# Kernel optimization log

Measured on AMD Instinct MI355X. Metric: run time of the kernel, lower is better.

## Reference

```python
import jax, jax.numpy as jnp
import numpy as np

B, C, N = 2, 512, 2048
HEADS, DIM_HEAD, SCALE = 16, 64, 8.0
H_DIM = HEADS * DIM_HEAD
EPS = 1e-12  # F.normalize default eps


def setup_inputs() -> dict:
    key = jax.random.key(0)
    ks = jax.random.split(key, 5)
    x = jax.random.normal(ks[0], (B, C, N), dtype=jnp.float32)
    Wqkv = jax.random.normal(ks[1], (3 * H_DIM, C), dtype=jnp.float32) * (1.0 / np.sqrt(C))
    q_scale = jnp.ones((DIM_HEAD,), dtype=jnp.float32)
    k_scale = jnp.ones((DIM_HEAD,), dtype=jnp.float32)
    Wout = jax.random.normal(ks[2], (C, H_DIM), dtype=jnp.float32) * (1.0 / np.sqrt(H_DIM))
    bout = jax.random.normal(ks[3], (C,), dtype=jnp.float32) * 0.01
    return {"x": x, "Wqkv": Wqkv, "q_scale": q_scale, "k_scale": k_scale,
            "Wout": Wout, "bout": bout}


def _l2norm(t):
    # F.normalize(t, dim=-1): t / max(||t||, eps)
    n = jnp.sqrt(jnp.sum(t * t, axis=-1, keepdims=True))
    return t / jnp.maximum(n, EPS)


def reference(x, Wqkv, q_scale, k_scale, Wout, bout):
    # 1x1 conv == pointwise matmul over channel dim
    qkv = jnp.einsum('oc,bcn->bon', Wqkv, x)              # [B, 3*H_DIM, N]
    q, k, v = jnp.split(qkv, 3, axis=1)
    # unflatten channels -> [B, H, D, N]
    def to_heads(t):
        return t.reshape(B, HEADS, DIM_HEAD, N)
    q, k, v = map(to_heads, (q, k, v))
    # cosine attention: l2-normalize q,k over head dim, apply learned per-dim scales
    q = _l2norm(q.transpose(0, 1, 3, 2)) * q_scale        # [B, H, N, D]
    k = _l2norm(k.transpose(0, 1, 3, 2)) * k_scale        # [B, H, N, D]
    sim = jnp.einsum('bhid,bhjd->bhij', q, k) * SCALE     # [B, H, N, N]
    attn = jax.nn.softmax(sim, axis=-1)
    out = jnp.einsum('bhij,bhdj->bhid', attn, v)          # [B, H, N, D]
    out = out.transpose(0, 1, 3, 2).reshape(B, H_DIM, N)  # b h n d -> b (h d) n
    return jnp.einsum('oc,bcn->bon', Wout, out) + bout[None, :, None]
```

## Files before the change

### kernel.cpp

```cpp
#include <hip/hip_runtime.h>
#include <hip/hip_bf16.h>

#define BATCH 2
#define CCH   512
#define NSEQ  2048
#define HEADS 16
#define DHEAD 64
#define HDIM  1024
#define ODIM  3072
#define QK_PRESCALE 11.541560327111707f

typedef short short4v __attribute__((ext_vector_type(4)));
typedef short short8 __attribute__((ext_vector_type(8)));
typedef float float4v __attribute__((ext_vector_type(4)));

__device__ __forceinline__ unsigned short f2bf(float f) {
    unsigned int u = __float_as_uint(f);
    return (unsigned short)((u + 0x7FFFu + ((u >> 16) & 1u)) >> 16);
}
__device__ __forceinline__ unsigned short f2bf_fast(float f) {
    return (unsigned short)((__float_as_uint(f) + 0x8000u) >> 16);
}
__device__ __forceinline__ float fexp2(float x) {
#if __has_builtin(__builtin_amdgcn_exp2f)
    return __builtin_amdgcn_exp2f(x);
#else
    return exp2f(x);
#endif
}

typedef __attribute__((address_space(1))) const void* as1_cvp;
typedef __attribute__((address_space(3))) void* as3_vp;
__device__ __forceinline__ void cp16(const void* g, void* l) {
    __builtin_amdgcn_global_load_lds((as1_cvp)g, (as3_vp)l, 16, 0, 0);
}

__global__ __launch_bounds__(256) void k_prep(
    const float* __restrict__ Wqkv, const float* __restrict__ Wout,
    const float* __restrict__ x,
    const float* __restrict__ qs, const float* __restrict__ ks,
    unsigned short* __restrict__ Wqkvb, unsigned short* __restrict__ Woutb,
    unsigned short* __restrict__ xt, float* __restrict__ M) {
    const int bx = blockIdx.x;
    if (bx < 2048) {
        if (bx == 0 && threadIdx.x < 64) {
            int lane = threadIdx.x;
            float p = fabsf(qs[lane] * ks[lane]);
#pragma unroll
            for (int off = 1; off < 64; off <<= 1) p = fmaxf(p, __shfl_xor(p, off));
            if (lane == 0) *M = QK_PRESCALE * p;
        }
        int i4 = (bx * 256 + threadIdx.x) * 4;
        const float* src; unsigned short* dst; int idx;
        if (i4 < ODIM * CCH) { src = Wqkv; dst = Wqkvb; idx = i4; }
        else { src = Wout; dst = Woutb; idx = i4 - ODIM * CCH; }
        float4 v = *(const float4*)(src + idx);
        ushort4 o;
        o.x = f2bf(v.x); o.y = f2bf(v.y); o.z = f2bf(v.z); o.w = f2bf(v.w);
        *(ushort4*)(dst + idx) = o;
        return;
    }
    __shared__ unsigned short t[64][65];
    const int fx = bx - 2048;
    const int n0 = (fx & 31) * 64;
    const int c0 = ((fx >> 5) & 7) * 64;
    const int b  = fx >> 8;
    const int tr = threadIdx.x >> 6, tc = threadIdx.x & 63;
    const float* xs = x + (size_t)b * CCH * NSEQ;
    unsigned short* xd = xt + (size_t)b * NSEQ * CCH;
#pragma unroll
    for (int r = 0; r < 16; ++r) {
        int c = r * 4 + tr;
        t[c][tc] = f2bf(xs[(size_t)(c0 + c) * NSEQ + n0 + tc]);
    }
    __syncthreads();
#pragma unroll
    for (int r = 0; r < 16; ++r) {
        int n = r * 4 + tr;
        xd[(size_t)(n0 + n) * CCH + c0 + tc] = t[tc][n];
    }
}

__global__ __launch_bounds__(256) void k_gemm_qkv(
    const unsigned short* __restrict__ W, const unsigned short* __restrict__ xt,
    const float* __restrict__ qs, const float* __restrict__ ks,
    unsigned short* __restrict__ qh, unsigned short* __restrict__ kh,
    unsigned short* __restrict__ vb) {
    constexpr int K = CCH, N = NSEQ;
    __shared__ __align__(16) short smem[2 * 128 * 64];
    short* lsA = smem;
    short* lsB = smem + 128 * 64;
    const int tid = threadIdx.x, wave = tid >> 6, lane = tid & 63;
    const int l15 = lane & 15, quad = lane >> 4;
    const int n0 = blockIdx.x * 128, m0 = blockIdx.y * 128, z = blockIdx.z;
    const short* Ab = (const short*)W + (size_t)m0 * K;
    const short* Bb = (const short*)xt + ((size_t)z * N + n0) * K;
    const int wm = wave >> 1, wn = wave & 1;
    const int cswz = (((tid & 7) ^ ((tid >> 3) & 7))) * 8;
    const int sw7 = (l15 & 7);

    float4v acc[4][4];
#pragma unroll
    for (int i = 0; i < 4; ++i)
#pragma unroll
        for (int j = 0; j < 4; ++j) acc[i][j] = (float4v){0.f, 0.f, 0.f, 0.f};

    for (int k0 = 0; k0 < K; k0 += 64) {
#pragma unroll
        for (int it = 0; it < 4; ++it) {
            int row = it * 32 + (tid >> 3);
            cp16(Ab + (size_t)row * K + k0 + cswz, &lsA[it * 2048 + wave * 512]);
            cp16(Bb + (size_t)row * K + k0 + cswz, &lsB[it * 2048 + wave * 512]);
        }
        __syncthreads();
        short8 af[4][2], bfr[4][2];
#pragma unroll
        for (int t = 0; t < 4; ++t)
#pragma unroll
            for (int kk = 0; kk < 2; ++kk) {
                af[t][kk]  = *(const short8*)&lsA[(wm * 64 + t * 16 + l15) * 64 + ((kk * 4 + quad) ^ sw7) * 8];
                bfr[t][kk] = *(const short8*)&lsB[(wn * 64 + t * 16 + l15) * 64 + ((kk * 4 + quad) ^ sw7) * 8];
            }
#pragma unroll
        for (int mt = 0; mt < 4; ++mt)
#pragma unroll
            for (int nt = 0; nt < 4; ++nt) {
                acc[mt][nt] = __builtin_amdgcn_mfma_f32_16x16x32_bf16(af[mt][0], bfr[nt][0], acc[mt][nt], 0, 0, 0);
                acc[mt][nt] = __builtin_amdgcn_mfma_f32_16x16x32_bf16(af[mt][1], bfr[nt][1], acc[mt][nt], 0, 0, 0);
            }
        __syncthreads();
    }

    const int co   = (m0 + wm * 64) >> 6;
    const int part = co >> 4;
    const int h    = co & 15;
    const int bh   = z * HEADS + h;
    short* myT = smem + wave * 4096;

    if (part < 2) {
        float inv[4];
#pragma unroll
        for (int nt = 0; nt < 4; ++nt) {
            float ss = 0.f;
#pragma unroll
            for (int mt = 0; mt < 4; ++mt)
#pragma unroll
                for (int r = 0; r < 4; ++r) ss += acc[mt][nt][r] * acc[mt][nt][r];
            ss += __shfl_xor(ss, 16);
            ss += __shfl_xor(ss, 32);
            inv[nt] = 1.0f / fmaxf(sqrtf(ss), 1e-12f);
        }
        const float* sc = part ? ks : qs;
        const float csc = part ? 1.0f : QK_PRESCALE;
#pragma unroll
        for (int mt = 0; mt < 4; ++mt) {
            const int db = mt * 16 + quad * 4;
            float4 s4 = *(const float4*)(sc + db);
            s4.x *= csc; s4.y *= csc; s4.z *= csc; s4.w *= csc;
#pragma unroll
            for (int nt = 0; nt < 4; ++nt) {
                int nl = nt * 16 + l15;
                short4v o;
                o.x = (short)f2bf(acc[mt][nt][0] * inv[nt] * s4.x);
                o.y = (short)f2bf(acc[mt][nt][1] * inv[nt] * s4.y);
                o.z = (short)f2bf(acc[mt][nt][2] * inv[nt] * s4.z);
                o.w = (short)f2bf(acc[mt][nt][3] * inv[nt] * s4.w);
                *(short4v*)&myT[nl * 64 + (((db >> 3) ^ (nl & 7)) << 3) + (db & 7)] = o;
            }
        }
        unsigned short* dst = (part ? kh : qh) + (size_t)bh * NSEQ * DHEAD
                              + (size_t)(n0 + wn * 64) * DHEAD;
#pragma unroll
        for (int pass = 0; pass < 8; ++pass) {
            int nl = pass * 8 + (lane >> 3), c = lane & 7;
            short8 vv = *(const short8*)&myT[nl * 64 + ((c ^ (nl & 7)) << 3)];
            *(short8*)&dst[(size_t)nl * DHEAD + c * 8] = vv;
        }
    } else {
#pragma unroll
        for (int mt = 0; mt < 4; ++mt)
#pragma unroll
            for (int nt = 0; nt < 4; ++nt) {
                int nl = nt * 16 + l15;
                int swc = nl >> 3, swo = nl & 7;
#pragma unroll
                for (int r = 0; r < 4; ++r) {
                    int d = mt * 16 + quad * 4 + r;
                    myT[d * 64 + ((swc ^ (d & 7)) << 3) + swo] = (short)f2bf(acc[mt][nt][r]);
                }
            }
        unsigned short* dst = vb + (size_t)bh * DHEAD * NSEQ + n0 + wn * 64;
#pragma unroll
        for (int pass = 0; pass < 8; ++pass) {
            int d = pass * 8 + (lane >> 3), c = lane & 7;
            short8 vv = *(const short8*)&myT[d * 64 + ((c ^ (d & 7)) << 3)];
            *(short8*)&dst[(size_t)d * NSEQ + c * 8] = vv;
        }
    }
}

__global__ __launch_bounds__(256, 2) void k_attn(
    const unsigned short* __restrict__ qh, const unsigned short* __restrict__ kh,
    const unsigned short* __restrict__ vb,
    unsigned short* __restrict__ aot, const float* __restrict__ Mptr) {
    __shared__ __align__(16) short Kt[2][64 * 64];
    __shared__ __align__(16) short Vt[2][64 * 64];
    __shared__ __align__(16) short Pt[128 * 64];
    const int tid = threadIdx.x, wave = tid >> 6, lane = tid & 63;
    const int l15 = lane & 15, quad = lane >> 4, q8 = quad * 8;
    const int flat = blockIdx.x;
    const int xcd = flat & 7, idx = flat >> 3;
    const int bh = xcd * 4 + (idx >> 4);
    const int i0 = (idx & 15) * 128;
    const int b = bh >> 4, h = bh & 15;
    const float Ms = *Mptr;
    const float4v mInit = (float4v){-Ms, -Ms, -Ms, -Ms};
    const int cswz = (((tid & 7) ^ ((tid >> 3) & 7))) * 8;
    const int sw7 = (l15 & 7);
    const int srow = tid >> 3;

    short8 qf[2][2];
    {
        const short* qb = (const short*)qh + ((size_t)bh * NSEQ + i0 + wave * 32) * DHEAD;
#pragma unroll
        for (int mt = 0; mt < 2; ++mt) {
            qf[mt][0] = *(const short8*)&qb[(mt * 16 + l15) * DHEAD + q8];
            qf[mt][1] = *(const short8*)&qb[(mt * 16 + l15) * DHEAD + 32 + q8];
        }
    }

    float4v of[2][4];
#pragma unroll
    for (int mt = 0; mt < 2; ++mt)
#pragma unroll
        for (int dt = 0; dt < 4; ++dt) of[mt][dt] = (float4v){0.f, 0.f, 0.f, 0.f};
    float l_acc[2][4];
#pragma unroll
    for (int mt = 0; mt < 2; ++mt)
#pragma unroll
        for (int r = 0; r < 4; ++r) l_acc[mt][r] = 0.f;

    const short* kbase = (const short*)kh + (size_t)bh * NSEQ * DHEAD;
    const short* vbase = (const short*)vb + (size_t)bh * DHEAD * NSEQ;

#pragma unroll
    for (int it = 0; it < 2; ++it) {
        int row = it * 32 + srow;
        cp16(kbase + (size_t)row * DHEAD + cswz, &Kt[0][it * 2048 + wave * 512]);
        cp16(vbase + (size_t)row * NSEQ + cswz, &Vt[0][it * 2048 + wave * 512]);
    }
    __syncthreads();

    int buf = 0;
    for (int j0 = 0; j0 < NSEQ; j0 += 64) {
        if (j0 + 64 < NSEQ) {
            int nb = buf ^ 1;
#pragma unroll
            for (int it = 0; it < 2; ++it) {
                int row = it * 32 + srow;
                cp16(kbase + (size_t)(j0 + 64 + row) * DHEAD + cswz, &Kt[nb][it * 2048 + wave * 512]);
                cp16(vbase + (size_t)row * NSEQ + j0 + 64 + cswz, &Vt[nb][it * 2048 + wave * 512]);
            }
        }

        float4v s[2][4];
#pragma unroll
        for (int nt = 0; nt < 4; ++nt) {
            short8 kf0 = *(const short8*)&Kt[buf][(nt * 16 + l15) * 64 + ((0 + quad) ^ sw7) * 8];
            short8 kf1 = *(const short8*)&Kt[buf][(nt * 16 + l15) * 64 + ((4 + quad) ^ sw7) * 8];
#pragma unroll
            for (int mt = 0; mt < 2; ++mt) {
                float4v zz = mInit;
                zz = __builtin_amdgcn_mfma_f32_16x16x32_bf16(qf[mt][0], kf0, zz, 0, 0, 0);
                zz = __builtin_amdgcn_mfma_f32_16x16x32_bf16(qf[mt][1], kf1, zz, 0, 0, 0);
                s[mt][nt] = zz;
            }
        }

#pragma unroll
        for (int mt = 0; mt < 2; ++mt)
#pragma unroll
            for (int r = 0; r < 4; ++r) {
                int prow = wave * 32 + mt * 16 + quad * 4 + r;
                int psw = prow & 7;
                float p0 = fexp2(s[mt][0][r]);
                float p1 = fexp2(s[mt][1][r]);
                float p2 = fexp2(s[mt][2][r]);
                float p3 = fexp2(s[mt][3][r]);
                l_acc[mt][r] += (p0 + p1) + (p2 + p3);
                Pt[prow * 64 + (((0 + (l15 >> 3)) ^ psw) * 8) + (l15 & 7)] = (short)f2bf_fast(p0);
                Pt[prow * 64 + (((2 + (l15 >> 3)) ^ psw) * 8) + (l15 & 7)] = (short)f2bf_fast(p1);
                Pt[prow * 64 + (((4 + (l15 >> 3)) ^ psw) * 8) + (l15 & 7)] = (short)f2bf_fast(p2);
                Pt[prow * 64 + (((6 + (l15 >> 3)) ^ psw) * 8) + (l15 & 7)] = (short)f2bf_fast(p3);
            }

        short8 af0[2], af1[2];
#pragma unroll
        for (int mt = 0; mt < 2; ++mt) {
            int arow = wave * 32 + mt * 16 + l15;
            af0[mt] = *(const short8*)&Pt[arow * 64 + ((0 + quad) ^ sw7) * 8];
            af1[mt] = *(const short8*)&Pt[arow * 64 + ((4 + quad) ^ sw7) * 8];
        }
#pragma unroll
        for (int dt = 0; dt < 4; ++dt) {
            short8 vf0 = *(const short8*)&Vt[buf][(dt * 16 + l15) * 64 + ((0 + quad) ^ sw7) * 8];
            short8 vf1 = *(const short8*)&Vt[buf][(dt * 16 + l15) * 64 + ((4 + quad) ^ sw7) * 8];
#pragma unroll
            for (int mt = 0; mt < 2; ++mt) {
                of[mt][dt] = __builtin_amdgcn_mfma_f32_16x16x32_bf16(af0[mt], vf0, of[mt][dt], 0, 0, 0);
                of[mt][dt] = __builtin_amdgcn_mfma_f32_16x16x32_bf16(af1[mt], vf1, of[mt][dt], 0, 0, 0);
            }
        }

        __syncthreads();
        buf ^= 1;
    }

#pragma unroll
    for (int mt = 0; mt < 2; ++mt)
#pragma unroll
        for (int r = 0; r < 4; ++r) {
            float l = l_acc[mt][r];
            l += __shfl_xor(l, 1); l += __shfl_xor(l, 2);
            l += __shfl_xor(l, 4); l += __shfl_xor(l, 8);
            l_acc[mt][r] = 1.0f / fmaxf(l, 1e-30f);
        }

#pragma unroll
    for (int mt = 0; mt < 2; ++mt) {
        unsigned short* ob = aot + ((size_t)b * NSEQ + i0 + wave * 32 + mt * 16) * HDIM + h * DHEAD;
#pragma unroll
        for (int dt = 0; dt < 4; ++dt)
#pragma unroll
            for (int r = 0; r < 4; ++r)
                ob[(size_t)(quad * 4 + r) * HDIM + dt * 16 + l15] = f2bf(of[mt][dt][r] * l_acc[mt][r]);
    }
}

__global__ __launch_bounds__(256) void k_gemm_out(
    const unsigned short* __restrict__ W, const unsigned short* __restrict__ aot,
    const float* __restrict__ bias, float* __restrict__ out) {
    constexpr int K = HDIM, N = NSEQ, M = CCH;
    __shared__ __align__(16) short lsA[64 * 64];
    __shared__ __align__(16) short lsB[64 * 64];
    const int tid = threadIdx.x, wave = tid >> 6, lane = tid & 63;
    const int l15 = lane & 15, quad = lane >> 4;
    const int n0 = blockIdx.x * 64, m0 = blockIdx.y * 64, z = blockIdx.z;
    const short* Ab = (const short*)W + (size_t)m0 * K;
    const short* Bb = (const short*)aot + ((size_t)z * N + n0) * K;
    const int wm = wave >> 1, wn = wave & 1;
    const int cswz = (((tid & 7) ^ ((tid >> 3) & 7))) * 8;
    const int sw7 = (l15 & 7);

    float4v acc[2][2];
#pragma unroll
    for (int i = 0; i < 2; ++i)
#pragma unroll
        for (int j = 0; j < 2; ++j) acc[i][j] = (float4v){0.f, 0.f, 0.f, 0.f};

    for (int k0 = 0; k0 < K; k0 += 64) {
        {
            int row = tid >> 3;
            cp16(Ab + (size_t)row * K + k0 + cswz, &lsA[wave * 512]);
            cp16(Ab + (size_t)(row + 32) * K + k0 + cswz, &lsA[2048 + wave * 512]);
            cp16(Bb + (size_t)row * K + k0 + cswz, &lsB[wave * 512]);
            cp16(Bb + (size_t)(row + 32) * K + k0 + cswz, &lsB[2048 + wave * 512]);
        }
        __syncthreads();
        short8 af[2][2], bfr[2][2];
#pragma unroll
        for (int t = 0; t < 2; ++t)
#pragma unroll
            for (int kk = 0; kk < 2; ++kk) {
                af[t][kk]  = *(const short8*)&lsA[(wm * 32 + t * 16 + l15) * 64 + ((kk * 4 + quad) ^ sw7) * 8];
                bfr[t][kk] = *(const short8*)&lsB[(wn * 32 + t * 16 + l15) * 64 + ((kk * 4 + quad) ^ sw7) * 8];
            }
#pragma unroll
        for (int mt = 0; mt < 2; ++mt)
#pragma unroll
            for (int nt = 0; nt < 2; ++nt) {
                acc[mt][nt] = __builtin_amdgcn_mfma_f32_16x16x32_bf16(af[mt][0], bfr[nt][0], acc[mt][nt], 0, 0, 0);
                acc[mt][nt] = __builtin_amdgcn_mfma_f32_16x16x32_bf16(af[mt][1], bfr[nt][1], acc[mt][nt], 0, 0, 0);
            }
        __syncthreads();
    }
    float* Co = out + (size_t)z * M * N;
#pragma unroll
    for (int mt = 0; mt < 2; ++mt)
#pragma unroll
        for (int nt = 0; nt < 2; ++nt) {
            int mrow = m0 + wm * 32 + mt * 16 + quad * 4;
#pragma unroll
            for (int r = 0; r < 4; ++r) {
                int mr = mrow + r;
                int nc = n0 + wn * 32 + nt * 16 + l15;
                Co[(size_t)mr * N + nc] = acc[mt][nt][r] + bias[mr];
            }
        }
}

extern "C" void kernel_launch(void* const* d_in, const int* in_sizes, int n_in,
                              void* d_out, int out_size, void* d_ws, size_t ws_size,
                              hipStream_t stream) {
    const float* x = nullptr; const float* Wqkv = nullptr;
    const float* qs = nullptr; const float* ks = nullptr;
    const float* Wout = nullptr; const float* bout = nullptr;
    for (int i = 0; i < n_in; ++i) {
        switch (in_sizes[i]) {
            case BATCH * CCH * NSEQ: x    = (const float*)d_in[i]; break;
            case ODIM * CCH:         Wqkv = (const float*)d_in[i]; break;
            case CCH * HDIM:         Wout = (const float*)d_in[i]; break;
            case CCH:                bout = (const float*)d_in[i]; break;
            case DHEAD: if (!qs) qs = (const float*)d_in[i]; else ks = (const float*)d_in[i]; break;
            default: break;
        }
    }
    float* y = (float*)d_out;

    char* ws = (char*)d_ws;
    float*          Mbuf  = (float*)(ws + 0);
    unsigned short* Wqkvb = (unsigned short*)(ws + 4096);
    unsigned short* Woutb = (unsigned short*)(ws + 3149824);
    unsigned short* xt    = (unsigned short*)(ws + 4198400);
    unsigned short* qh    = (unsigned short*)(ws + 8392704);
    unsigned short* kh    = (unsigned short*)(ws + 16781312);
    unsigned short* vb    = (unsigned short*)(ws + 25169920);
    unsigned short* aot   = (unsigned short*)(ws + 33558528);

    k_prep<<<dim3(2048 + 512), 256, 0, stream>>>(Wqkv, Wout, x, qs, ks, Wqkvb, Woutb, xt, Mbuf);
    k_gemm_qkv<<<dim3(NSEQ / 128, ODIM / 128, BATCH), 256, 0, stream>>>(Wqkvb, xt, qs, ks, qh, kh, vb);
    k_attn<<<dim3(512), 256, 0, stream>>>(qh, kh, vb, aot, Mbuf);
    k_gemm_out<<<dim3(NSEQ / 64, CCH / 64, BATCH), 256, 0, stream>>>(Woutb, aot, bout, y);
}
```

Before: 161.4 us.

## Keep P in registers via transposed S=K·Q^T and enlarge output GEMM M-tile

The attention loop now computes the transposed score tile (K as A operand, Q as B operand), so each lane's exponentiated probabilities already sit in the B-operand layout for the P·V MFMA. This removes the LDS round-trip through the Pt buffer and its extra reads and writes. It also permutes K rows so the accumulator layout matches, and writes the output as vectorized ushort4 stores. Separately, the output projection GEMM tile grows from 64 to 128 rows in M, giving each wave more MFMAs per LDS load at the cost of more registers and half as many blocks.

```diff
diff --git a/kernel.cpp b/kernel.cpp
--- a/kernel.cpp
+++ b/kernel.cpp
@@ -205,7 +205,6 @@
     unsigned short* __restrict__ aot, const float* __restrict__ Mptr) {
     __shared__ __align__(16) short Kt[2][64 * 64];
     __shared__ __align__(16) short Vt[2][64 * 64];
-    __shared__ __align__(16) short Pt[128 * 64];
     const int tid = threadIdx.x, wave = tid >> 6, lane = tid & 63;
     const int l15 = lane & 15, quad = lane >> 4, q8 = quad * 8;
     const int flat = blockIdx.x;
@@ -216,29 +215,26 @@
     const float Ms = *Mptr;
     const float4v mInit = (float4v){-Ms, -Ms, -Ms, -Ms};
     const int cswz = (((tid & 7) ^ ((tid >> 3) & 7))) * 8;
-    const int sw7 = (l15 & 7);
     const int srow = tid >> 3;
+    const int ar0 = (l15 >> 2) * 8 + (l15 & 3);
+    const int ar1 = ar0 + 4;
 
     short8 qf[2][2];
     {
         const short* qb = (const short*)qh + ((size_t)bh * NSEQ + i0 + wave * 32) * DHEAD;
 #pragma unroll
-        for (int mt = 0; mt < 2; ++mt) {
-            qf[mt][0] = *(const short8*)&qb[(mt * 16 + l15) * DHEAD + q8];
-            qf[mt][1] = *(const short8*)&qb[(mt * 16 + l15) * DHEAD + 32 + q8];
+        for (int it = 0; it < 2; ++it) {
+            qf[it][0] = *(const short8*)&qb[(it * 16 + l15) * DHEAD + q8];
+            qf[it][1] = *(const short8*)&qb[(it * 16 + l15) * DHEAD + 32 + q8];
         }
     }
 
     float4v of[2][4];
 #pragma unroll
-    for (int mt = 0; mt < 2; ++mt)
-#pragma unroll
-        for (int dt = 0; dt < 4; ++dt) of[mt][dt] = (float4v){0.f, 0.f, 0.f, 0.f};
-    float l_acc[2][4];
-#pragma unroll
-    for (int mt = 0; mt < 2; ++mt)
-#pragma unroll
-        for (int r = 0; r < 4; ++r) l_acc[mt][r] = 0.f;
+    for (int it = 0; it < 2; ++it)
+#pragma unroll
+        for (int dt = 0; dt < 4; ++dt) of[it][dt] = (float4v){0.f, 0.f, 0.f, 0.f};
+    float l_acc[2] = {0.f, 0.f};
 
     const short* kbase = (const short*)kh + (size_t)bh * NSEQ * DHEAD;
     const short* vbase = (const short*)vb + (size_t)bh * DHEAD * NSEQ;
@@ -263,52 +259,39 @@
             }
         }
 
-        float4v s[2][4];
-#pragma unroll
-        for (int nt = 0; nt < 4; ++nt) {
-            short8 kf0 = *(const short8*)&Kt[buf][(nt * 16 + l15) * 64 + ((0 + quad) ^ sw7) * 8];
-            short8 kf1 = *(const short8*)&Kt[buf][(nt * 16 + l15) * 64 + ((4 + quad) ^ sw7) * 8];
-#pragma unroll
-            for (int mt = 0; mt < 2; ++mt) {
-                float4v zz = mInit;
-                zz = __builtin_amdgcn_mfma_f32_16x16x32_bf16(qf[mt][0], kf0, zz, 0, 0, 0);
-                zz = __builtin_amdgcn_mfma_f32_16x16x32_bf16(qf[mt][1], kf1, zz, 0, 0, 0);
-                s[mt][nt] = zz;
-            }
-        }
-
-#pragma unroll
-        for (int mt = 0; mt < 2; ++mt)
-#pragma unroll
-            for (int r = 0; r < 4; ++r) {
-                int prow = wave * 32 + mt * 16 + quad * 4 + r;
-                int psw = prow & 7;
-                float p0 = fexp2(s[mt][0][r]);
-                float p1 = fexp2(s[mt][1][r]);
-                float p2 = fexp2(s[mt][2][r]);
-                float p3 = fexp2(s[mt][3][r]);
-                l_acc[mt][r] += (p0 + p1) + (p2 + p3);
-                Pt[prow * 64 + (((0 + (l15 >> 3)) ^ psw) * 8) + (l15 & 7)] = (short)f2bf_fast(p0);
-                Pt[prow * 64 + (((2 + (l15 >> 3)) ^ psw) * 8) + (l15 & 7)] = (short)f2bf_fast(p1);
-                Pt[prow * 64 + (((4 + (l15 >> 3)) ^ psw) * 8) + (l15 & 7)] = (short)f2bf_fast(p2);
-                Pt[prow * 64 + (((6 + (l15 >> 3)) ^ psw) * 8) + (l15 & 7)] = (short)f2bf_fast(p3);
-            }
-
-        short8 af0[2], af1[2];
-#pragma unroll
-        for (int mt = 0; mt < 2; ++mt) {
-            int arow = wave * 32 + mt * 16 + l15;
-            af0[mt] = *(const short8*)&Pt[arow * 64 + ((0 + quad) ^ sw7) * 8];
-            af1[mt] = *(const short8*)&Pt[arow * 64 + ((4 + quad) ^ sw7) * 8];
-        }
-#pragma unroll
-        for (int dt = 0; dt < 4; ++dt) {
-            short8 vf0 = *(const short8*)&Vt[buf][(dt * 16 + l15) * 64 + ((0 + quad) ^ sw7) * 8];
-            short8 vf1 = *(const short8*)&Vt[buf][(dt * 16 + l15) * 64 + ((4 + quad) ^ sw7) * 8];
-#pragma unroll
-            for (int mt = 0; mt < 2; ++mt) {
-                of[mt][dt] = __builtin_amdgcn_mfma_f32_16x16x32_bf16(af0[mt], vf0, of[mt][dt], 0, 0, 0);
-                of[mt][dt] = __builtin_amdgcn_mfma_f32_16x16x32_bf16(af1[mt], vf1, of[mt][dt], 0, 0, 0);
+#pragma unroll
+        for (int ch = 0; ch < 2; ++ch) {
+            short8 pb[2];
+#pragma unroll
+            for (int t = 0; t < 2; ++t) {
+                const int arow = ch * 32 + (t ? ar1 : ar0);
+                const int asw = arow & 7;
+                const short* kr = &Kt[buf][arow * 64];
+                short8 kf0 = *(const short8*)&kr[((0 + quad) ^ asw) * 8];
+                short8 kf1 = *(const short8*)&kr[((4 + quad) ^ asw) * 8];
+#pragma unroll
+                for (int it = 0; it < 2; ++it) {
+                    float4v s = mInit;
+                    s = __builtin_amdgcn_mfma_f32_16x16x32_bf16(kf0, qf[it][0], s, 0, 0, 0);
+                    s = __builtin_amdgcn_mfma_f32_16x16x32_bf16(kf1, qf[it][1], s, 0, 0, 0);
+                    float p0 = fexp2(s[0]);
+                    float p1 = fexp2(s[1]);
+                    float p2 = fexp2(s[2]);
+                    float p3 = fexp2(s[3]);
+                    l_acc[it] += (p0 + p1) + (p2 + p3);
+                    pb[it][t * 4 + 0] = (short)f2bf_fast(p0);
+                    pb[it][t * 4 + 1] = (short)f2bf_fast(p1);
+                    pb[it][t * 4 + 2] = (short)f2bf_fast(p2);
+                    pb[it][t * 4 + 3] = (short)f2bf_fast(p3);
+                }
+            }
+#pragma unroll
+            for (int dt = 0; dt < 4; ++dt) {
+                int vrow = dt * 16 + l15;
+                int vsw = vrow & 7;
+                short8 av = *(const short8*)&Vt[buf][vrow * 64 + (((ch * 4 + quad) ^ vsw)) * 8];
+                of[0][dt] = __builtin_amdgcn_mfma_f32_16x16x32_bf16(av, pb[0], of[0][dt], 0, 0, 0);
+                of[1][dt] = __builtin_amdgcn_mfma_f32_16x16x32_bf16(av, pb[1], of[1][dt], 0, 0, 0);
             }
         }
 
@@ -317,23 +300,21 @@
     }
 
 #pragma unroll
-    for (int mt = 0; mt < 2; ++mt)
-#pragma unroll
-        for (int r = 0; r < 4; ++r) {
-            float l = l_acc[mt][r];
-            l += __shfl_xor(l, 1); l += __shfl_xor(l, 2);
-            l += __shfl_xor(l, 4); l += __shfl_xor(l, 8);
-            l_acc[mt][r] = 1.0f / fmaxf(l, 1e-30f);
-        }
-
-#pragma unroll
-    for (int mt = 0; mt < 2; ++mt) {
-        unsigned short* ob = aot + ((size_t)b * NSEQ + i0 + wave * 32 + mt * 16) * HDIM + h * DHEAD;
-#pragma unroll
-        for (int dt = 0; dt < 4; ++dt)
-#pragma unroll
-            for (int r = 0; r < 4; ++r)
-                ob[(size_t)(quad * 4 + r) * HDIM + dt * 16 + l15] = f2bf(of[mt][dt][r] * l_acc[mt][r]);
+    for (int it = 0; it < 2; ++it) {
+        float l = l_acc[it];
+        l += __shfl_xor(l, 16);
+        l += __shfl_xor(l, 32);
+        float inv = 1.0f / fmaxf(l, 1e-30f);
+        unsigned short* ob = aot + ((size_t)b * NSEQ + i0 + wave * 32 + it * 16 + l15) * HDIM + h * DHEAD;
+#pragma unroll
+        for (int dt = 0; dt < 4; ++dt) {
+            ushort4 o;
+            o.x = f2bf(of[it][dt][0] * inv);
+            o.y = f2bf(of[it][dt][1] * inv);
+            o.z = f2bf(of[it][dt][2] * inv);
+            o.w = f2bf(of[it][dt][3] * inv);
+            *(ushort4*)&ob[dt * 16 + quad * 4] = o;
+        }
     }
 }
 
@@ -341,42 +322,49 @@
     const unsigned short* __restrict__ W, const unsigned short* __restrict__ aot,
     const float* __restrict__ bias, float* __restrict__ out) {
     constexpr int K = HDIM, N = NSEQ, M = CCH;
-    __shared__ __align__(16) short lsA[64 * 64];
+    __shared__ __align__(16) short lsA[128 * 64];
     __shared__ __align__(16) short lsB[64 * 64];
     const int tid = threadIdx.x, wave = tid >> 6, lane = tid & 63;
     const int l15 = lane & 15, quad = lane >> 4;
-    const int n0 = blockIdx.x * 64, m0 = blockIdx.y * 64, z = blockIdx.z;
+    const int n0 = blockIdx.x * 64, m0 = blockIdx.y * 128, z = blockIdx.z;
     const short* Ab = (const short*)W + (size_t)m0 * K;
     const short* Bb = (const short*)aot + ((size_t)z * N + n0) * K;
     const int wm = wave >> 1, wn = wave & 1;
     const int cswz = (((tid & 7) ^ ((tid >> 3) & 7))) * 8;
     const int sw7 = (l15 & 7);
-
-    float4v acc[2][2];
-#pragma unroll
-    for (int i = 0; i < 2; ++i)
+    const int srow = tid >> 3;
+
+    float4v acc[4][2];
+#pragma unroll
+    for (int i = 0; i < 4; ++i)
 #pragma unroll
         for (int j = 0; j < 2; ++j) acc[i][j] = (float4v){0.f, 0.f, 0.f, 0.f};
 
     for (int k0 = 0; k0 < K; k0 += 64) {
-        {
-            int row = tid >> 3;
-            cp16(Ab + (size_t)row * K + k0 + cswz, &lsA[wave * 512]);
-            cp16(Ab + (size_t)(row + 32) * K + k0 + cswz, &lsA[2048 + wave * 512]);
-            cp16(Bb + (size_t)row * K + k0 + cswz, &lsB[wave * 512]);
-            cp16(Bb + (size_t)(row + 32) * K + k0 + cswz, &lsB[2048 + wave * 512]);
+#pragma unroll
+        for (int it = 0; it < 4; ++it) {
+            int row = it * 32 + srow;
+            cp16(Ab + (size_t)row * K + k0 + cswz, &lsA[it * 2048 + wave * 512]);
+        }
+#pragma unroll
+        for (int it = 0; it < 2; ++it) {
+            int row = it * 32 + srow;
+            cp16(Bb + (size_t)row * K + k0 + cswz, &lsB[it * 2048 + wave * 512]);
         }
         __syncthreads();
-        short8 af[2][2], bfr[2][2];
+        short8 af[4][2], bfr[2][2];
+#pragma unroll
+        for (int t = 0; t < 4; ++t)
+#pragma unroll
+            for (int kk = 0; kk < 2; ++kk)
+                af[t][kk] = *(const short8*)&lsA[(wm * 64 + t * 16 + l15) * 64 + ((kk * 4 + quad) ^ sw7) * 8];
 #pragma unroll
         for (int t = 0; t < 2; ++t)
 #pragma unroll
-            for (int kk = 0; kk < 2; ++kk) {
-                af[t][kk]  = *(const short8*)&lsA[(wm * 32 + t * 16 + l15) * 64 + ((kk * 4 + quad) ^ sw7) * 8];
+            for (int kk = 0; kk < 2; ++kk)
                 bfr[t][kk] = *(const short8*)&lsB[(wn * 32 + t * 16 + l15) * 64 + ((kk * 4 + quad) ^ sw7) * 8];
-            }
-#pragma unroll
-        for (int mt = 0; mt < 2; ++mt)
+#pragma unroll
+        for (int mt = 0; mt < 4; ++mt)
 #pragma unroll
             for (int nt = 0; nt < 2; ++nt) {
                 acc[mt][nt] = __builtin_amdgcn_mfma_f32_16x16x32_bf16(af[mt][0], bfr[nt][0], acc[mt][nt], 0, 0, 0);
@@ -386,10 +374,10 @@
     }
     float* Co = out + (size_t)z * M * N;
 #pragma unroll
-    for (int mt = 0; mt < 2; ++mt)
+    for (int mt = 0; mt < 4; ++mt)
 #pragma unroll
         for (int nt = 0; nt < 2; ++nt) {
-            int mrow = m0 + wm * 32 + mt * 16 + quad * 4;
+            int mrow = m0 + wm * 64 + mt * 16 + quad * 4;
 #pragma unroll
             for (int r = 0; r < 4; ++r) {
                 int mr = mrow + r;
@@ -430,5 +418,5 @@
     k_prep<<<dim3(2048 + 512), 256, 0, stream>>>(Wqkv, Wout, x, qs, ks, Wqkvb, Woutb, xt, Mbuf);
     k_gemm_qkv<<<dim3(NSEQ / 128, ODIM / 128, BATCH), 256, 0, stream>>>(Wqkvb, xt, qs, ks, qh, kh, vb);
     k_attn<<<dim3(512), 256, 0, stream>>>(qh, kh, vb, aot, Mbuf);
-    k_gemm_out<<<dim3(NSEQ / 64, CCH / 64, BATCH), 256, 0, stream>>>(Woutb, aot, bout, y);
-}
+    k_gemm_out<<<dim3(NSEQ / 64, CCH / 128, BATCH), 256, 0, stream>>>(Woutb, aot, bout, y);
+}
```

Result: faster. 153.9 us (-4.6%).
